# Performance work log

Hardware: AMD Instinct MI355X
Metric: run time of the kernel (lower is better)

## Reference

```python
import jax, jax.numpy as jnp
import numpy as np

EXP_SCALING = 10.0
N_HEAD = 16
KEY_SCALE_MAX = float(np.log(2 ** 16 - 1))


def setup_inputs() -> dict:
    key = jax.random.key(0)
    k1, k2, k3, k4 = jax.random.split(key, 4)
    B, T, C = 8, 2048, 1024
    nh = N_HEAD
    x = jax.random.normal(k1, (B, T, C), dtype=jnp.float32)
    Wk_weight = jax.random.normal(k2, (C, C), dtype=jnp.float32) * (1.0 / np.sqrt(C))
    # faithful to torch init: linspace(0.5, 5, nh)/10 and ones/10
    leaky_key_beta = (jnp.linspace(0.5, 5.0, nh, dtype=jnp.float32) / EXP_SCALING).reshape(1, nh, 1, 1)
    key_scale = jnp.ones((1, nh, 1, 1), dtype=jnp.float32) / EXP_SCALING
    return {"x": x, "Wk_weight": Wk_weight, "leaky_key_beta": leaky_key_beta,
            "key_scale": key_scale, "scale_pow": 1}


def reference(x, Wk_weight, leaky_key_beta, key_scale, scale_pow):
    B, T, C = x.shape
    nh = N_HEAD
    hs = C // nh
    # W_k projection + head split (the torch transpose/view dance is the standard split)
    k = (x @ Wk_weight.T).reshape(B, T, nh, hs).transpose(0, 2, 1, 3)  # (B, nh, T, hs)
    # LeakyAvg: coef[t, s] = exp(-(t - s) * beta_h) for s <= t, else 0
    beta = jnp.abs(leaky_key_beta).reshape(nh, 1, 1) * EXP_SCALING  # (nh, 1, 1)
    idx = jnp.arange(T)
    diff = idx[:, None] - idx[None, :]                # (T, T), >=0 below diag
    mask = diff >= 0
    diff_c = jnp.where(mask, diff, 0).astype(x.dtype)
    coef = jnp.exp(-diff_c * beta) * mask.astype(x.dtype)  # (nh, T, T) lower-triangular
    k = jnp.einsum('hts,bhsd->bhtd', coef, k)         # causal decay-weighted sum
    # L2 normalize along head dim
    k = k / (jnp.linalg.norm(k, axis=-1, keepdims=True) + 1e-10)
    # per-head learned scale, clamped in log-space
    scale = jnp.exp(jnp.minimum(scale_pow * EXP_SCALING * key_scale, KEY_SCALE_MAX))
    return k * scale
```

## Files before the change

### kernel.cpp

```cpp
#include <hip/hip_runtime.h>
#include <hip/hip_bf16.h>
#include <stdint.h>

#define B_SZ   8
#define T_SEQ  2048
#define C_DIM  1024
#define NH     16
#define HS     64
#define M_DIM  (B_SZ * T_SEQ)
#define EXP_SC 10.0f
#define KS_MAX 11.090339630053288f

typedef _Float16 f16;
typedef __attribute__((ext_vector_type(8))) _Float16 f16x8;
typedef __attribute__((ext_vector_type(4))) float f32x4;

__global__ void cast_two(const float* __restrict__ xin, f16* __restrict__ xout, int n8x,
                         const float* __restrict__ win, f16* __restrict__ wout, int n8w) {
  int stride = gridDim.x * blockDim.x;
  int t0 = blockIdx.x * blockDim.x + threadIdx.x;
  for (int i = t0; i < n8x; i += stride) {
    const float* p = xin + (size_t)i * 8;
    float4 a = *(const float4*)p;
    float4 b = *(const float4*)(p + 4);
    f16x8 o;
    o[0] = (f16)a.x; o[1] = (f16)a.y; o[2] = (f16)a.z; o[3] = (f16)a.w;
    o[4] = (f16)b.x; o[5] = (f16)b.y; o[6] = (f16)b.z; o[7] = (f16)b.w;
    *(f16x8*)(xout + (size_t)i * 8) = o;
  }
  for (int i = t0; i < n8w; i += stride) {
    const float* p = win + (size_t)i * 8;
    float4 a = *(const float4*)p;
    float4 b = *(const float4*)(p + 4);
    f16x8 o;
    o[0] = (f16)a.x; o[1] = (f16)a.y; o[2] = (f16)a.z; o[3] = (f16)a.w;
    o[4] = (f16)b.x; o[5] = (f16)b.y; o[6] = (f16)b.z; o[7] = (f16)b.w;
    *(f16x8*)(wout + (size_t)i * 8) = o;
  }
}

__device__ __forceinline__ void gl_lds16(const f16* g, const f16* l) {
  __builtin_amdgcn_global_load_lds(
      (const __attribute__((address_space(1))) void*)(uintptr_t)(const void*)g,
      (__attribute__((address_space(3))) void*)(uintptr_t)(const void*)l,
      16, 0, 0);
}

__global__ __launch_bounds__(512, 2)
void gemm_bt_f16_8p(const f16* __restrict__ A,
                    const f16* __restrict__ Bt,
                    float* __restrict__ C) {
  __shared__ f16 As[2][2][128 * 64];
  __shared__ f16 Bs[2][2][128 * 64];

  const int tid = threadIdx.x;
  const int w = tid >> 6, l = tid & 63;
  const int wm = w >> 2, wn = w & 3;

  const int q = blockIdx.x;
  const int wgid = (q & 7) * 32 + (q >> 3);
  const int bm = wgid >> 2;
  const int bn = wgid & 3;

  const int srow = l >> 3;
  const int sswz = (((l & 7) ^ srow)) << 3;
  const size_t a_lane = (size_t)(bm * 256 + w * 8 + srow) * C_DIM + sswz;
  const size_t b_lane = (size_t)(bn * 256 + w * 8 + srow) * C_DIM + sswz;
  const int lds_w = w * 512;

  const int fr = l & 15;
  const int fk = l >> 4;
  const int ck0 = ((fk) ^ (l & 7)) << 3;
  const int ck1 = ((4 + fk) ^ (l & 7)) << 3;

  const f32x4 zero = {0.f, 0.f, 0.f, 0.f};
  f32x4 acc[8][4];
#pragma unroll
  for (int i = 0; i < 8; ++i)
#pragma unroll
    for (int j = 0; j < 4; ++j) acc[i][j] = zero;

  f16x8 af[4][2], b0[2][2], b1[2][2];

#define STAGE_A(buf, kt) do {                                                \
    size_t ko = (size_t)(kt) * 64;                                           \
    gl_lds16(A + a_lane + ko,                         &As[buf][0][lds_w]);        \
    gl_lds16(A + a_lane + ko + (size_t) 64 * C_DIM,   &As[buf][0][lds_w + 4096]); \
    gl_lds16(A + a_lane + ko + (size_t)128 * C_DIM,   &As[buf][1][lds_w]);        \
    gl_lds16(A + a_lane + ko + (size_t)192 * C_DIM,   &As[buf][1][lds_w + 4096]); \
  } while (0)
#define STAGE_B(buf, kt) do {                                                \
    size_t ko = (size_t)(kt) * 64;                                           \
    gl_lds16(Bt + b_lane + ko,                        &Bs[buf][0][lds_w]);        \
    gl_lds16(Bt + b_lane + ko + (size_t) 64 * C_DIM,  &Bs[buf][0][lds_w + 4096]); \
    gl_lds16(Bt + b_lane + ko + (size_t)128 * C_DIM,  &Bs[buf][1][lds_w]);        \
    gl_lds16(Bt + b_lane + ko + (size_t)192 * C_DIM,  &Bs[buf][1][lds_w + 4096]); \
  } while (0)

#define MFMA16(mi, ni, BREG) do {                                            \
    _Pragma("unroll") for (int kk = 0; kk < 2; ++kk)                         \
    _Pragma("unroll") for (int i = 0; i < 4; ++i)                            \
    _Pragma("unroll") for (int j = 0; j < 2; ++j)                            \
      acc[(mi)*4 + i][(ni)*2 + j] = __builtin_amdgcn_mfma_f32_16x16x32_f16(  \
          af[i][kk], BREG[j][kk], acc[(mi)*4 + i][(ni)*2 + j], 0, 0, 0);     \
  } while (0)

  STAGE_A(0, 0); STAGE_B(0, 0);
  __syncthreads();

  for (int kt = 0; kt < 16; ++kt) {
    const int cur = kt & 1;
    const f16* Ab = &As[cur][wm][0];
    const f16* Bb = &Bs[cur][wn >> 1][(wn & 1) * 4096];

#pragma unroll
    for (int i = 0; i < 4; ++i) {
      af[i][0] = *(const f16x8*)(Ab + (i * 16 + fr) * 64 + ck0);
      af[i][1] = *(const f16x8*)(Ab + (i * 16 + fr) * 64 + ck1);
    }
#pragma unroll
    for (int j = 0; j < 2; ++j) {
      b0[j][0] = *(const f16x8*)(Bb + (j * 16 + fr) * 64 + ck0);
      b0[j][1] = *(const f16x8*)(Bb + (j * 16 + fr) * 64 + ck1);
    }
    if (kt < 15) STAGE_A(cur ^ 1, kt + 1);
    __builtin_amdgcn_s_barrier();
    asm volatile("s_waitcnt lgkmcnt(0)" ::: "memory");
    __builtin_amdgcn_s_setprio(1);
    MFMA16(0, 0, b0);
    __builtin_amdgcn_s_setprio(0);
    __builtin_amdgcn_s_barrier();

#pragma unroll
    for (int j = 0; j < 2; ++j) {
      b1[j][0] = *(const f16x8*)(Bb + ((2 + j) * 16 + fr) * 64 + ck0);
      b1[j][1] = *(const f16x8*)(Bb + ((2 + j) * 16 + fr) * 64 + ck1);
    }
    if (kt < 15) STAGE_B(cur ^ 1, kt + 1);
    __builtin_amdgcn_s_barrier();
    asm volatile("s_waitcnt lgkmcnt(0)" ::: "memory");
    __builtin_amdgcn_s_setprio(1);
    MFMA16(0, 1, b1);
    __builtin_amdgcn_s_setprio(0);
    __builtin_amdgcn_s_barrier();

#pragma unroll
    for (int i = 0; i < 4; ++i) {
      af[i][0] = *(const f16x8*)(Ab + (64 + i * 16 + fr) * 64 + ck0);
      af[i][1] = *(const f16x8*)(Ab + (64 + i * 16 + fr) * 64 + ck1);
    }
    __builtin_amdgcn_s_barrier();
    asm volatile("s_waitcnt lgkmcnt(0)" ::: "memory");
    __builtin_amdgcn_s_setprio(1);
    MFMA16(1, 1, b1);
    __builtin_amdgcn_s_setprio(0);
    __builtin_amdgcn_s_barrier();

    __builtin_amdgcn_s_setprio(1);
    MFMA16(1, 0, b0);
    __builtin_amdgcn_s_setprio(0);
    asm volatile("s_waitcnt vmcnt(0)" ::: "memory");
    __builtin_amdgcn_s_barrier();
  }
#undef STAGE_A
#undef STAGE_B
#undef MFMA16

  const int orow0 = bm * 256 + wm * 128 + (l >> 4) * 4;
  const int ocol0 = bn * 256 + wn * 64 + (l & 15);
#pragma unroll
  for (int i = 0; i < 8; ++i)
#pragma unroll
    for (int j = 0; j < 4; ++j)
#pragma unroll
      for (int r = 0; r < 4; ++r)
        C[(size_t)(orow0 + i * 16 + r) * C_DIM + ocol0 + j * 16] = acc[i][j][r];
}

__global__ __launch_bounds__(256)
void scan_norm(const float* __restrict__ kbuf,
               const float* __restrict__ beta_p,
               const float* __restrict__ ks_p,
               const int* __restrict__ sp_p,
               float* __restrict__ out) {
  const int l = threadIdx.x & 63;
  const int gw = blockIdx.x * 4 + (threadIdx.x >> 6);
  const int c = gw & 31;
  const int h = (gw >> 5) & 15;
  const int b = gw >> 9;

  const float beta = fabsf(beta_p[h]) * EXP_SC;
  const float a = expf(-beta);
  const float sp = (float)sp_p[0];
  const float scale = expf(fminf(sp * EXP_SC * ks_p[h], KS_MAX));

  const float* kp = kbuf + (size_t)b * T_SEQ * C_DIM + h * HS + l;
  float* op = out + ((size_t)(b * NH + h) * T_SEQ) * HS + l;

  const int t0 = c * 64;
  float y = 0.f;
  int s = (t0 >= 64) ? (t0 - 64) : 0;
#pragma unroll 8
  for (; s < t0; ++s)
    y = fmaf(a, y, kp[(size_t)s * C_DIM]);

#pragma unroll 4
  for (int t = t0; t < t0 + 64; ++t) {
    y = fmaf(a, y, kp[(size_t)t * C_DIM]);
    float sq = y * y;
#pragma unroll
    for (int m = 1; m < 64; m <<= 1)
      sq += __shfl_xor(sq, m, 64);
    float nrm = sqrtf(sq) + 1e-10f;
    op[(size_t)t * HS] = y * (scale / nrm);
  }
}

extern "C" void kernel_launch(void* const* d_in, const int* in_sizes, int n_in,
                              void* d_out, int out_size, void* d_ws, size_t ws_size,
                              hipStream_t stream) {
  const float* x      = (const float*)d_in[0];
  const float* Wk     = (const float*)d_in[1];
  const float* beta   = (const float*)d_in[2];
  const float* kscale = (const float*)d_in[3];
  const int*   spow   = (const int*)d_in[4];
  float* out = (float*)d_out;

  f16* x_h = (f16*)d_ws;
  f16* W_h = x_h + (size_t)M_DIM * C_DIM;
  float* kbuf = (float*)(W_h + (size_t)C_DIM * C_DIM);

  cast_two<<<2048, 256, 0, stream>>>(x, x_h, (M_DIM * C_DIM) / 8,
                                     Wk, W_h, (C_DIM * C_DIM) / 8);
  gemm_bt_f16_8p<<<dim3((M_DIM / 256) * (C_DIM / 256)), 512, 0, stream>>>(x_h, W_h, kbuf);
  scan_norm<<<1024, 256, 0, stream>>>(kbuf, beta, kscale, spow, out);
}
```

Measured before the change: 198.2 us.

## Store GEMM output as f16 in head-major layout and pack scan to two channels per lane

The GEMM epilogue now writes the projected keys as f16 directly in (B, nh, T, hs) layout instead of as an fp32 row-major buffer. This halves the intermediate traffic and makes the scan's reads contiguous. The scan kernel gives each lane two channels with paired f16 loads and float2 stores, packs two segments per wavefront with a 32-lane reduction, and splits the 64-step warmup into two independent 32-step chains joined with a32. The risks are f16 rounding of the intermediate keys and scattered 2-byte stores in the GEMM epilogue.

```diff
diff --git a/kernel.cpp b/kernel.cpp
--- a/kernel.cpp
+++ b/kernel.cpp
@@ -13,6 +13,7 @@
 
 typedef _Float16 f16;
 typedef __attribute__((ext_vector_type(8))) _Float16 f16x8;
+typedef __attribute__((ext_vector_type(2))) _Float16 f16x2;
 typedef __attribute__((ext_vector_type(4))) float f32x4;
 
 __global__ void cast_two(const float* __restrict__ xin, f16* __restrict__ xout, int n8x,
@@ -49,7 +50,7 @@
 __global__ __launch_bounds__(512, 2)
 void gemm_bt_f16_8p(const f16* __restrict__ A,
                     const f16* __restrict__ Bt,
-                    float* __restrict__ C) {
+                    f16* __restrict__ KB) {
   __shared__ f16 As[2][2][128 * 64];
   __shared__ f16 Bs[2][2][128 * 64];
 
@@ -166,53 +167,75 @@
 #undef STAGE_B
 #undef MFMA16
 
-  const int orow0 = bm * 256 + wm * 128 + (l >> 4) * 4;
-  const int ocol0 = bn * 256 + wn * 64 + (l & 15);
+  const int b   = bm >> 3;
+  const int tb  = (bm & 7) * 256 + wm * 128 + (l >> 4) * 4;
+  const int h   = bn * 4 + wn;
+  f16* kb = KB + ((size_t)(b * NH + h) * T_SEQ + tb) * HS + (l & 15);
 #pragma unroll
   for (int i = 0; i < 8; ++i)
 #pragma unroll
     for (int j = 0; j < 4; ++j)
 #pragma unroll
       for (int r = 0; r < 4; ++r)
-        C[(size_t)(orow0 + i * 16 + r) * C_DIM + ocol0 + j * 16] = acc[i][j][r];
+        kb[(size_t)(i * 16 + r) * HS + j * 16] = (f16)acc[i][j][r];
 }
 
 __global__ __launch_bounds__(256)
-void scan_norm(const float* __restrict__ kbuf,
-               const float* __restrict__ beta_p,
-               const float* __restrict__ ks_p,
-               const int* __restrict__ sp_p,
-               float* __restrict__ out) {
+void scan_norm2(const f16* __restrict__ kb,
+                const float* __restrict__ beta_p,
+                const float* __restrict__ ks_p,
+                const int* __restrict__ sp_p,
+                float* __restrict__ out) {
   const int l = threadIdx.x & 63;
+  const int g = l & 31;
   const int gw = blockIdx.x * 4 + (threadIdx.x >> 6);
-  const int c = gw & 31;
-  const int h = (gw >> 5) & 15;
-  const int b = gw >> 9;
+  const int sid = gw * 2 + (l >> 5);
+  const int c = sid & 31;
+  const int h = (sid >> 5) & 15;
+  const int b = sid >> 9;
 
   const float beta = fabsf(beta_p[h]) * EXP_SC;
   const float a = expf(-beta);
+  float a2 = a * a, a4 = a2 * a2, a8 = a4 * a4, a16 = a8 * a8;
+  const float a32 = a16 * a16;
   const float sp = (float)sp_p[0];
   const float scale = expf(fminf(sp * EXP_SC * ks_p[h], KS_MAX));
 
-  const float* kp = kbuf + (size_t)b * T_SEQ * C_DIM + h * HS + l;
-  float* op = out + ((size_t)(b * NH + h) * T_SEQ) * HS + l;
+  const f16* kp = kb + (size_t)(b * NH + h) * T_SEQ * HS + 2 * g;
+  float* op = out + (size_t)(b * NH + h) * T_SEQ * HS + 2 * g;
 
   const int t0 = c * 64;
-  float y = 0.f;
-  int s = (t0 >= 64) ? (t0 - 64) : 0;
-#pragma unroll 8
-  for (; s < t0; ++s)
-    y = fmaf(a, y, kp[(size_t)s * C_DIM]);
+  float y0 = 0.f, y1 = 0.f;
+  if (t0) {
+    float p0 = 0.f, p1 = 0.f, q0 = 0.f, q1 = 0.f;
+#pragma unroll 4
+    for (int s = t0 - 64; s < t0 - 32; ++s) {
+      f16x2 v = *(const f16x2*)(kp + (size_t)s * HS);
+      p0 = fmaf(a, p0, (float)v[0]);
+      p1 = fmaf(a, p1, (float)v[1]);
+    }
+#pragma unroll 4
+    for (int s = t0 - 32; s < t0; ++s) {
+      f16x2 v = *(const f16x2*)(kp + (size_t)s * HS);
+      q0 = fmaf(a, q0, (float)v[0]);
+      q1 = fmaf(a, q1, (float)v[1]);
+    }
+    y0 = fmaf(p0, a32, q0);
+    y1 = fmaf(p1, a32, q1);
+  }
 
 #pragma unroll 4
   for (int t = t0; t < t0 + 64; ++t) {
-    y = fmaf(a, y, kp[(size_t)t * C_DIM]);
-    float sq = y * y;
-#pragma unroll
-    for (int m = 1; m < 64; m <<= 1)
+    f16x2 v = *(const f16x2*)(kp + (size_t)t * HS);
+    y0 = fmaf(a, y0, (float)v[0]);
+    y1 = fmaf(a, y1, (float)v[1]);
+    float sq = fmaf(y0, y0, y1 * y1);
+#pragma unroll
+    for (int m = 1; m < 32; m <<= 1)
       sq += __shfl_xor(sq, m, 64);
-    float nrm = sqrtf(sq) + 1e-10f;
-    op[(size_t)t * HS] = y * (scale / nrm);
+    float inv = scale / (sqrtf(sq) + 1e-10f);
+    float2 o; o.x = y0 * inv; o.y = y1 * inv;
+    *(float2*)(op + (size_t)t * HS) = o;
   }
 }
 
@@ -228,10 +251,10 @@
 
   f16* x_h = (f16*)d_ws;
   f16* W_h = x_h + (size_t)M_DIM * C_DIM;
-  float* kbuf = (float*)(W_h + (size_t)C_DIM * C_DIM);
+  f16* kb  = W_h + (size_t)C_DIM * C_DIM;
 
   cast_two<<<2048, 256, 0, stream>>>(x, x_h, (M_DIM * C_DIM) / 8,
                                      Wk, W_h, (C_DIM * C_DIM) / 8);
-  gemm_bt_f16_8p<<<dim3((M_DIM / 256) * (C_DIM / 256)), 512, 0, stream>>>(x_h, W_h, kbuf);
-  scan_norm<<<1024, 256, 0, stream>>>(kbuf, beta, kscale, spow, out);
-}
+  gemm_bt_f16_8p<<<dim3((M_DIM / 256) * (C_DIM / 256)), 512, 0, stream>>>(x_h, W_h, kb);
+  scan_norm2<<<512, 256, 0, stream>>>(kb, beta, kscale, spow, out);
+}
```

Result: no change. 198.6 us (+0.2%).
